# Performance work log

Measured on AMD Instinct MI355X. Metric: run time of the kernel, lower is better.

Reference implementation:

```python
import jax, jax.numpy as jnp
import numpy as np

DIM = 384
HEADS = 12
HEAD_DIM = DIM // HEADS
SCALE = HEAD_DIM ** -0.5
HIDDEN = 4 * DIM
EPS = 1e-5


def _dwconv(x, w, b):
    # depthwise 3x3 conv, NCHW, kernel [C,1,3,3], groups=C
    y = jax.lax.conv_general_dilated(
        x, w, window_strides=(1, 1), padding='SAME',
        dimension_numbers=('NCHW', 'OIHW', 'NCHW'),
        feature_group_count=x.shape[1])
    return y + b[None, :, None, None]


def _layernorm(x, g, b):
    mu = jnp.mean(x, axis=-1, keepdims=True)
    var = jnp.mean(jnp.square(x - mu), axis=-1, keepdims=True)
    return (x - mu) * jax.lax.rsqrt(var + EPS) * g + b


def setup_inputs() -> dict:
    key = jax.random.key(0)
    ks = jax.random.split(key, 10)
    s = 0.02
    inp = {
        'x': jax.random.normal(ks[0], (32, DIM, 28, 28), dtype=jnp.float32),
        'cpe1_w': jax.random.normal(ks[1], (DIM, 1, 3, 3), dtype=jnp.float32) * s,
        'cpe1_b': jnp.zeros((DIM,), jnp.float32),
        'norm1_g': jnp.ones((DIM,), jnp.float32),
        'norm1_b': jnp.zeros((DIM,), jnp.float32),
        'qkv_w': jax.random.normal(ks[2], (3 * DIM, DIM), dtype=jnp.float32) * s,
        'proj_w': jax.random.normal(ks[3], (DIM, DIM), dtype=jnp.float32) * s,
        'proj_b': jnp.zeros((DIM,), jnp.float32),
        'cpe2_w': jax.random.normal(ks[4], (DIM, 1, 3, 3), dtype=jnp.float32) * s,
        'cpe2_b': jnp.zeros((DIM,), jnp.float32),
        'norm2_g': jnp.ones((DIM,), jnp.float32),
        'norm2_b': jnp.zeros((DIM,), jnp.float32),
        'fc1_w': jax.random.normal(ks[5], (HIDDEN, DIM), dtype=jnp.float32) * s,
        'fc1_b': jnp.zeros((HIDDEN,), jnp.float32),
        'fc2_w': jax.random.normal(ks[6], (DIM, HIDDEN), dtype=jnp.float32) * s,
        'fc2_b': jnp.zeros((DIM,), jnp.float32),
    }
    return inp


def reference(x, cpe1_w, cpe1_b, norm1_g, norm1_b, qkv_w, proj_w, proj_b,
              cpe2_w, cpe2_b, norm2_g, norm2_b, fc1_w, fc1_b, fc2_w, fc2_b):
    B, C, H, W = x.shape
    N = H * W
    # cpe1: depthwise conv residual (act = Identity)
    x = x + _dwconv(x, cpe1_w, cpe1_b)
    x = jnp.transpose(x.reshape(B, C, N), (0, 2, 1))  # [B, N, C]

    # channel attention
    cur = _layernorm(x, norm1_g, norm1_b)
    qkv = cur @ qkv_w.T  # [B, N, 3C]
    qkv = qkv.reshape(B, N, 3, HEADS, HEAD_DIM)
    q = qkv[:, :, 0]  # [B, N, h, d]
    k = qkv[:, :, 1] * SCALE
    v = qkv[:, :, 2]
    # attn = k^T @ v over tokens: [B, h, d, d]
    attn = jnp.einsum('bnhd,bnhe->bhde', k, v)
    attn = jax.nn.softmax(attn, axis=-1)
    # out[n,d] = sum_e attn[d,e] * q[n,e]
    out = jnp.einsum('bhde,bnhe->bnhd', attn, q).reshape(B, N, C)
    cur = out @ proj_w.T + proj_b
    x = x + cur

    # cpe2
    x = jnp.transpose(x, (0, 2, 1)).reshape(B, C, H, W)
    x = x + _dwconv(x, cpe2_w, cpe2_b)

    # MLP
    x = jnp.transpose(x.reshape(B, C, N), (0, 2, 1))  # [B, N, C]
    y = _layernorm(x, norm2_g, norm2_b)
    y = jax.nn.gelu(y @ fc1_w.T + fc1_b, approximate=False)
    y = y @ fc2_w.T + fc2_b
    x = x + y
    return jnp.transpose(x, (0, 2, 1)).reshape(B, C, H, W)
```

## Files before the change

kernel.cpp:

```cpp
#include <hip/hip_runtime.h>
#include <hip/hip_bf16.h>

#define CDIM 384
#define NHEADS 12
#define HDIM 32
#define HIDDEN 1536
#define BBATCH 32
#define HH 28
#define WW 28
#define NTOK 784
#define BN (BBATCH * NTOK)
#define LN_EPS 1e-5f
#define ATT_SCALE 0.17677669529663687f
#define YTILES 196
#define PERXCD 25

typedef __hip_bfloat16 bf16;
typedef __attribute__((ext_vector_type(8))) short bf16x8;
typedef __attribute__((ext_vector_type(4))) float f32x4;

__device__ __forceinline__ void stf(float* p, float v) { *p = v; }
__device__ __forceinline__ void stf(bf16* p, float v) { *p = __float2bfloat16(v); }

__device__ __forceinline__ short f2bs(float v) {
    bf16 t = __float2bfloat16(v);
    return *reinterpret_cast<short*>(&t);
}

__device__ __forceinline__ float bf2f(unsigned short u) {
    return __uint_as_float(((unsigned)u) << 16);
}

__device__ __forceinline__ float gelu_f(float x) {
    float u = x * (0.7978845608f + 0.0356774081f * x * x);
    float e = __expf(-2.f * u);
    return x / (1.f + e);
}

__device__ __forceinline__ void gload16(const void* g, void* l) {
    __builtin_amdgcn_global_load_lds(
        (const __attribute__((address_space(1))) unsigned int*)g,
        (__attribute__((address_space(3))) unsigned int*)l, 16, 0, 0);
}

__global__ __launch_bounds__(256) void prep_k(
    const float* __restrict__ w0, const float* __restrict__ w1,
    const float* __restrict__ w2, const float* __restrict__ w3,
    bf16* __restrict__ dst, const float* __restrict__ cw,
    float* __restrict__ cwt)
{
    int blk = blockIdx.x;
    if (blk >= 6912) {
        int i = (blk - 6912) * 256 + threadIdx.x;
        if (i < 9 * CDIM) {
            int k = i / CDIM, c = i % CDIM;
            cwt[i] = cw[c * 9 + k];
        }
        return;
    }
    int i = blk * 256 + threadIdx.x;
    const float* src; int off;
    if (i < 442368)       { src = w0; off = i; }
    else if (i < 589824)  { src = w1; off = i - 442368; }
    else if (i < 1179648) { src = w2; off = i - 589824; }
    else                  { src = w3; off = i - 1179648; }
    dst[i] = __float2bfloat16(src[off]);
}

__global__ __launch_bounds__(256) void cpe1_tr_v3(
    const float* __restrict__ x, const float* __restrict__ w,
    const float* __restrict__ bias, float* __restrict__ xt)
{
    __shared__ float sm[32][130];
    __shared__ float wls[32][10];
    __shared__ float bls[32];
    int b = blockIdx.z;
    int n0 = blockIdx.y * 64;
    int c0 = blockIdx.x * 32;
    int tid = threadIdx.x;
    int nf0 = (n0 - 32) >> 2;

    for (int i = tid; i < 288; i += 256) wls[i / 9][i % 9] = w[c0 * 9 + i];
    if (tid < 32) bls[tid] = bias[c0 + tid];

    const float4* xb = (const float4*)(x + ((size_t)b * CDIM + c0) * NTOK);
#pragma unroll
    for (int i = 0; i < 4; i++) {
        int q = tid + i * 256;
        int row = q >> 5, c4 = q & 31;
        int nf = nf0 + c4;
        float4 v = {0.f, 0.f, 0.f, 0.f};
        if ((unsigned)nf < (NTOK >> 2)) v = xb[(size_t)row * (NTOK >> 2) + nf];
        float2* p = (float2*)&sm[row][c4 * 4];
        p[0] = make_float2(v.x, v.y);
        p[1] = make_float2(v.z, v.w);
    }
    __syncthreads();

    int c = tid & 31;
    int tsub = tid >> 5;
    float wr[9];
#pragma unroll
    for (int k = 0; k < 9; k++) wr[k] = wls[c][k];
    float bb = bls[c];
    const float* s = sm[c];
#pragma unroll
    for (int it = 0; it < 8; it++) {
        int tok = it * 8 + tsub;
        int n = n0 + tok;
        if (n < NTOK) {
            int h = n / WW, wc = n % WW;
            bool hm = h > 0, hp = h < HH - 1, wm = wc > 0, wpv = wc < WW - 1;
            int l = 32 + tok;
            float a = wr[4] * s[l];
            if (hm)        a += wr[1] * s[l - WW];
            if (hp)        a += wr[7] * s[l + WW];
            if (wm)        a += wr[3] * s[l - 1];
            if (wpv)       a += wr[5] * s[l + 1];
            if (hm && wm)  a += wr[0] * s[l - WW - 1];
            if (hm && wpv) a += wr[2] * s[l - WW + 1];
            if (hp && wm)  a += wr[6] * s[l + WW - 1];
            if (hp && wpv) a += wr[8] * s[l + WW + 1];
            xt[((size_t)b * NTOK + n) * CDIM + c0 + c] = s[l] + a + bb;
        }
    }
}

__global__ __launch_bounds__(256) void ln1_k(
    const float* __restrict__ in, const float* __restrict__ g,
    const float* __restrict__ b, bf16* __restrict__ out)
{
    int tid = threadIdx.x;
    int l = tid & 31;
    size_t tok = (size_t)blockIdx.x * 8 + (tid >> 5);
    const float4* row = (const float4*)(in + tok * CDIM);
    float4 v[3];
    float s = 0.f;
#pragma unroll
    for (int j = 0; j < 3; j++) {
        v[j] = row[l + j * 32];
        s += v[j].x + v[j].y + v[j].z + v[j].w;
    }
#pragma unroll
    for (int off = 16; off >= 1; off >>= 1) s += __shfl_xor(s, off);
    float mu = s * (1.f / CDIM);
    float q = 0.f;
#pragma unroll
    for (int j = 0; j < 3; j++) {
        float dx = v[j].x - mu, dy = v[j].y - mu;
        float dz = v[j].z - mu, dw = v[j].w - mu;
        q += dx * dx + dy * dy + dz * dz + dw * dw;
    }
#pragma unroll
    for (int off = 16; off >= 1; off >>= 1) q += __shfl_xor(q, off);
    float rs = rsqrtf(q * (1.f / CDIM) + LN_EPS);
    const float4* g4 = (const float4*)g;
    const float4* b4 = (const float4*)b;
    ushort4* o4 = (ushort4*)(out + tok * CDIM);
#pragma unroll
    for (int j = 0; j < 3; j++) {
        int idx = l + j * 32;
        float4 gv = g4[idx], bv = b4[idx];
        ushort4 r;
        r.x = (unsigned short)f2bs((v[j].x - mu) * rs * gv.x + bv.x);
        r.y = (unsigned short)f2bs((v[j].y - mu) * rs * gv.y + bv.y);
        r.z = (unsigned short)f2bs((v[j].z - mu) * rs * gv.z + bv.z);
        r.w = (unsigned short)f2bs((v[j].w - mu) * rs * gv.w + bv.w);
        o4[idx] = r;
    }
}

__global__ __launch_bounds__(256) void cpe2_ln_fused(
    const float* __restrict__ xin, const float* __restrict__ wt,
    const float* __restrict__ cbias, const float* __restrict__ g,
    const float* __restrict__ b, float* __restrict__ x3,
    bf16* __restrict__ lnout)
{
    __shared__ float wts[9 * CDIM];
    int tid = threadIdx.x;
    for (int i = tid; i < 864; i += 256)
        ((float4*)wts)[i] = ((const float4*)wt)[i];
    __syncthreads();
    int l = tid & 31;
    size_t tok = (size_t)blockIdx.x * 8 + (tid >> 5);
    int n = (int)(tok % NTOK);
    int h = n / WW, wc = n % WW;
    bool hm = h > 0, hp = h < HH - 1, wm = wc > 0, wpv = wc < WW - 1;
    const float* row = xin + tok * CDIM;
    const float4* w4 = (const float4*)wts;
    float4 ctr[3], acc[3];
#pragma unroll
    for (int j = 0; j < 3; j++) {
        int idx = l + j * 32;
        ctr[j] = ((const float4*)row)[idx];
        float4 ww = w4[4 * 96 + idx];
        acc[j].x = ww.x * ctr[j].x; acc[j].y = ww.y * ctr[j].y;
        acc[j].z = ww.z * ctr[j].z; acc[j].w = ww.w * ctr[j].w;
    }
#define TAP(k, cond, dn)                                                     \
    if (cond) {                                                              \
        const float4* rp = (const float4*)(row + (dn) * CDIM);               \
        _Pragma("unroll")                                                    \
        for (int j = 0; j < 3; j++) {                                        \
            int idx = l + j * 32;                                            \
            float4 vv = rp[idx];                                             \
            float4 ww = w4[(k) * 96 + idx];                                  \
            acc[j].x = fmaf(ww.x, vv.x, acc[j].x);                           \
            acc[j].y = fmaf(ww.y, vv.y, acc[j].y);                           \
            acc[j].z = fmaf(ww.z, vv.z, acc[j].z);                           \
            acc[j].w = fmaf(ww.w, vv.w, acc[j].w);                           \
        }                                                                    \
    }
    TAP(0, hm && wm,   -WW - 1)
    TAP(1, hm,         -WW)
    TAP(2, hm && wpv,  -WW + 1)
    TAP(3, wm,         -1)
    TAP(5, wpv,        1)
    TAP(6, hp && wm,   WW - 1)
    TAP(7, hp,         WW)
    TAP(8, hp && wpv,  WW + 1)
#undef TAP
    float s = 0.f;
    float4 val[3];
    float4* x3r = (float4*)(x3 + tok * CDIM);
#pragma unroll
    for (int j = 0; j < 3; j++) {
        int idx = l + j * 32;
        float4 cb = ((const float4*)cbias)[idx];
        val[j].x = ctr[j].x + acc[j].x + cb.x;
        val[j].y = ctr[j].y + acc[j].y + cb.y;
        val[j].z = ctr[j].z + acc[j].z + cb.z;
        val[j].w = ctr[j].w + acc[j].w + cb.w;
        x3r[idx] = val[j];
        s += val[j].x + val[j].y + val[j].z + val[j].w;
    }
#pragma unroll
    for (int off = 16; off >= 1; off >>= 1) s += __shfl_xor(s, off);
    float mu = s * (1.f / CDIM);
    float q = 0.f;
#pragma unroll
    for (int j = 0; j < 3; j++) {
        float dx = val[j].x - mu, dy = val[j].y - mu;
        float dz = val[j].z - mu, dw = val[j].w - mu;
        q += dx * dx + dy * dy + dz * dz + dw * dw;
    }
#pragma unroll
    for (int off = 16; off >= 1; off >>= 1) q += __shfl_xor(q, off);
    float rs = rsqrtf(q * (1.f / CDIM) + LN_EPS);
    const float4* g4 = (const float4*)g;
    const float4* b4 = (const float4*)b;
    ushort4* o4 = (ushort4*)(lnout + tok * CDIM);
#pragma unroll
    for (int j = 0; j < 3; j++) {
        int idx = l + j * 32;
        float4 gv = g4[idx], bv = b4[idx];
        ushort4 r;
        r.x = (unsigned short)f2bs((val[j].x - mu) * rs * gv.x + bv.x);
        r.y = (unsigned short)f2bs((val[j].y - mu) * rs * gv.y + bv.y);
        r.z = (unsigned short)f2bs((val[j].z - mu) * rs * gv.z + bv.z);
        r.w = (unsigned short)f2bs((val[j].w - mu) * rs * gv.w + bv.w);
        o4[idx] = r;
    }
}

template <int ACT, bool RES, typename TO, bool OUTT, int K>
__global__ __launch_bounds__(256, 4) void gemm_mfma(
    const short* __restrict__ Abf, const short* __restrict__ Bw,
    const float* __restrict__ bias, const float* __restrict__ res,
    TO* __restrict__ Co, int M, int NX)
{
    int id = blockIdx.x;
    int xcd = id & 7, slot_ = id >> 3;
    int yloc = slot_ / NX, xx = slot_ - yloc * NX;
    int y = xcd * PERXCD + yloc;
    if (y >= YTILES) return;

    __shared__ __align__(16) short lds[16896];
    const int tid = threadIdx.x;
    const int wid = tid >> 6, lane = tid & 63;
    const int wrow = wid >> 1, wcol = wid & 1;
    const int quad = lane >> 4, lr = lane & 15;
    const int r0 = y * 128, m0 = xx * 128;

    const int srow = lane >> 2;
    const int sg   = (lane & 3) ^ ((lane >> 3) & 3);
    const short* gA = Abf + (size_t)(r0 + wid * 32 + srow) * K + sg * 8;
    const short* gB = Bw  + (size_t)(m0 + wid * 32 + srow) * K + sg * 8;

    auto stage = [&](int k0, int p) {
        short* lA = lds + p * 8192 + wid * 1024;
        short* lB = lds + p * 8192 + 4096 + wid * 1024;
#pragma unroll
        for (int k = 0; k < 2; k++) {
            gload16(gA + k0 + (size_t)k * 16 * K, lA + k * 512);
            gload16(gB + k0 + (size_t)k * 16 * K, lB + k * 512);
        }
    };

    const int slot = (quad ^ ((lr >> 1) & 3)) * 8;
    int fA[4], fB[4];
#pragma unroll
    for (int i = 0; i < 4; i++) {
        fA[i] = (wrow * 64 + i * 16 + lr) * 32 + slot;
        fB[i] = 4096 + (wcol * 64 + i * 16 + lr) * 32 + slot;
    }

    f32x4 acc[4][4] = {};

    stage(0, 0);
    int p = 0;
    for (int k0 = 0; k0 < K; k0 += 32) {
        __syncthreads();
        if (k0 + 32 < K) stage(k0 + 32, p ^ 1);
        const short* As = lds + p * 8192;
        bf16x8 av[4], bv[4];
#pragma unroll
        for (int i = 0; i < 4; i++) {
            av[i] = *(const bf16x8*)(As + fA[i]);
            bv[i] = *(const bf16x8*)(As + fB[i]);
        }
#pragma unroll
        for (int i = 0; i < 4; i++)
#pragma unroll
            for (int j = 0; j < 4; j++)
                acc[i][j] = __builtin_amdgcn_mfma_f32_16x16x32_bf16(
                    av[i], bv[j], acc[i][j], 0, 0, 0);
        p ^= 1;
    }

    if constexpr (OUTT) {
        float* Csf = (float*)lds;
        __syncthreads();
#pragma unroll
        for (int pass = 0; pass < 2; pass++) {
            if (wcol == pass) {
#pragma unroll
                for (int i = 0; i < 4; i++) {
                    int lrow = wrow * 64 + i * 16 + quad * 4;
#pragma unroll
                    for (int j = 0; j < 4; j++) {
                        int lcol = j * 16 + lr;
                        int gc = m0 + pass * 64 + lcol;
                        float bb = bias ? bias[gc] : 0.f;
#pragma unroll
                        for (int rr = 0; rr < 4; rr++) {
                            float v = acc[i][j][rr] + bb;
                            if (RES)
                                v += res[(size_t)(r0 + lrow + rr) * M + gc];
                            if (ACT == 1) v = gelu_f(v);
                            Csf[(lrow + rr) * 66 + lcol] = v;
                        }
                    }
                }
            }
            __syncthreads();
            int tok = tid & 127;
            int csel = tid >> 7;
            int gtok = r0 + tok;
            int bb2 = gtok / NTOK;
            int nn2 = gtok - bb2 * NTOK;
#pragma unroll
            for (int s = 0; s < 32; s++) {
                int cl = s * 2 + csel;
                int gcol = m0 + pass * 64 + cl;
                Co[((size_t)bb2 * CDIM + gcol) * NTOK + nn2] = Csf[tok * 66 + cl];
            }
            __syncthreads();
        }
    } else if constexpr (sizeof(TO) == 4) {
#pragma unroll
        for (int i = 0; i < 4; i++) {
            int gr = r0 + wrow * 64 + i * 16 + quad * 4;
#pragma unroll
            for (int j = 0; j < 4; j++) {
                int gc = m0 + wcol * 64 + j * 16 + lr;
                float bb = bias ? bias[gc] : 0.f;
#pragma unroll
                for (int rr = 0; rr < 4; rr++) {
                    size_t idx = (size_t)(gr + rr) * M + gc;
                    float v = acc[i][j][rr] + bb;
                    if (RES) v += res[idx];
                    if (ACT == 1) v = gelu_f(v);
                    stf((float*)&Co[idx], v);
                }
            }
        }
    } else {
        __syncthreads();
        short* Cs = lds;
#pragma unroll
        for (int i = 0; i < 4; i++) {
            int lrow = wrow * 64 + i * 16 + quad * 4;
#pragma unroll
            for (int j = 0; j < 4; j++) {
                int lcol = wcol * 64 + j * 16 + lr;
                float bb = bias ? bias[m0 + lcol] : 0.f;
#pragma unroll
                for (int rr = 0; rr < 4; rr++) {
                    float v = acc[i][j][rr] + bb;
                    if (ACT == 1) v = gelu_f(v);
                    Cs[(lrow + rr) * 132 + lcol] = f2bs(v);
                }
            }
        }
        __syncthreads();
        short* co = (short*)Co;
#pragma unroll
        for (int s = 0; s < 16; s++) {
            int row = s * 8 + (tid >> 5);
            int seg = tid & 31;
            uint2 vv = *(const uint2*)(Cs + row * 132 + seg * 4);
            *(uint2*)(co + (size_t)(r0 + row) * M + m0 + seg * 4) = vv;
        }
    }
}

__global__ __launch_bounds__(256) void attn_k(
    const bf16* __restrict__ qkv, float* __restrict__ attn)
{
    int bh = blockIdx.x;
    int b = bh / NHEADS, h = bh % NHEADS;
    __shared__ float ks[64][32];
    __shared__ float vs[64][32];
    __shared__ float sm[32][33];
    int tid = threadIdx.x;
    int d = tid >> 3, e0 = (tid & 7) * 4;
    int nn = tid >> 2, q8 = (tid & 3) * 8;
    float acc[4] = {0.f, 0.f, 0.f, 0.f};
    for (int n0 = 0; n0 < NTOK; n0 += 64) {
        int n = n0 + nn;
        float kv[8], vv[8];
        if (n < NTOK) {
            const unsigned short* base =
                (const unsigned short*)qkv + ((size_t)b * NTOK + n) * (3 * CDIM);
            uint4 kq = *(const uint4*)(base + CDIM + h * HDIM + q8);
            uint4 vq = *(const uint4*)(base + 2 * CDIM + h * HDIM + q8);
            const unsigned short* kp = (const unsigned short*)&kq;
            const unsigned short* vp = (const unsigned short*)&vq;
#pragma unroll
            for (int j = 0; j < 8; j++) {
                kv[j] = ATT_SCALE * bf2f(kp[j]);
                vv[j] = bf2f(vp[j]);
            }
        } else {
#pragma unroll
            for (int j = 0; j < 8; j++) { kv[j] = 0.f; vv[j] = 0.f; }
        }
        *(float4*)&ks[nn][q8]     = make_float4(kv[0], kv[1], kv[2], kv[3]);
        *(float4*)&ks[nn][q8 + 4] = make_float4(kv[4], kv[5], kv[6], kv[7]);
        *(float4*)&vs[nn][q8]     = make_float4(vv[0], vv[1], vv[2], vv[3]);
        *(float4*)&vs[nn][q8 + 4] = make_float4(vv[4], vv[5], vv[6], vv[7]);
        __syncthreads();
#pragma unroll 8
        for (int k = 0; k < 64; k++) {
            float kd = ks[k][d];
            float4 vv4 = *(const float4*)&vs[k][e0];
            acc[0] = fmaf(kd, vv4.x, acc[0]);
            acc[1] = fmaf(kd, vv4.y, acc[1]);
            acc[2] = fmaf(kd, vv4.z, acc[2]);
            acc[3] = fmaf(kd, vv4.w, acc[3]);
        }
        __syncthreads();
    }
#pragma unroll
    for (int j = 0; j < 4; j++) sm[d][e0 + j] = acc[j];
    __syncthreads();
    if (tid < 32) {
        float mx = -1e30f;
#pragma unroll
        for (int e = 0; e < 32; e++) mx = fmaxf(mx, sm[tid][e]);
        float ssum = 0.f;
        float ex[32];
#pragma unroll
        for (int e = 0; e < 32; e++) { ex[e] = expf(sm[tid][e] - mx); ssum += ex[e]; }
        float inv = 1.f / ssum;
        float* arow = attn + ((size_t)bh * 32 + tid) * 32;
#pragma unroll
        for (int e = 0; e < 32; e++) arow[e] = ex[e] * inv;
    }
}

__global__ __launch_bounds__(384) void apply_attn_k(
    const bf16* __restrict__ qkv, const float* __restrict__ attn,
    bf16* __restrict__ out)
{
    int b = blockIdx.x;
    int chunk = blockIdx.y;
    int tid = threadIdx.x;
    int h = tid >> 5;
    __shared__ float qs[8][CDIM];
    float at[32];
    const float4* ap = (const float4*)(attn + ((size_t)(b * NHEADS) * 32 + tid) * 32);
#pragma unroll
    for (int e4 = 0; e4 < 8; e4++) {
        float4 v = ap[e4];
        at[e4 * 4 + 0] = v.x; at[e4 * 4 + 1] = v.y;
        at[e4 * 4 + 2] = v.z; at[e4 * 4 + 3] = v.w;
    }
    int row8 = tid / 48;
    int seg = tid - row8 * 48;
    int nbase = chunk * 56;
    for (int t0 = 0; t0 < 56; t0 += 8) {
        __syncthreads();
        {
            int n = nbase + t0 + row8;
            const unsigned short* src =
                (const unsigned short*)qkv + ((size_t)b * NTOK + n) * (3 * CDIM) + seg * 8;
            uint4 qv = *(const uint4*)src;
            const unsigned short* qp = (const unsigned short*)&qv;
            *(float4*)&qs[row8][seg * 8] =
                make_float4(bf2f(qp[0]), bf2f(qp[1]), bf2f(qp[2]), bf2f(qp[3]));
            *(float4*)&qs[row8][seg * 8 + 4] =
                make_float4(bf2f(qp[4]), bf2f(qp[5]), bf2f(qp[6]), bf2f(qp[7]));
        }
        __syncthreads();
#pragma unroll
        for (int i = 0; i < 8; i++) {
            const float4* q4 = (const float4*)&qs[i][h * 32];
            float s = 0.f;
#pragma unroll
            for (int e4 = 0; e4 < 8; e4++) {
                float4 qv = q4[e4];
                s = fmaf(at[e4 * 4 + 0], qv.x, s);
                s = fmaf(at[e4 * 4 + 1], qv.y, s);
                s = fmaf(at[e4 * 4 + 2], qv.z, s);
                s = fmaf(at[e4 * 4 + 3], qv.w, s);
            }
            int n = nbase + t0 + i;
            out[((size_t)b * NTOK + n) * CDIM + tid] = __float2bfloat16(s);
        }
    }
}

extern "C" void kernel_launch(void* const* d_in, const int* in_sizes, int n_in,
                              void* d_out, int out_size, void* d_ws, size_t ws_size,
                              hipStream_t stream) {
    const float* x      = (const float*)d_in[0];
    const float* cpe1_w = (const float*)d_in[1];
    const float* cpe1_b = (const float*)d_in[2];
    const float* n1g    = (const float*)d_in[3];
    const float* n1b    = (const float*)d_in[4];
    const float* qkv_w  = (const float*)d_in[5];
    const float* proj_w = (const float*)d_in[6];
    const float* proj_b = (const float*)d_in[7];
    const float* cpe2_w = (const float*)d_in[8];
    const float* cpe2_b = (const float*)d_in[9];
    const float* n2g    = (const float*)d_in[10];
    const float* n2b    = (const float*)d_in[11];
    const float* fc1_w  = (const float*)d_in[12];
    const float* fc1_b  = (const float*)d_in[13];
    const float* fc2_w  = (const float*)d_in[14];
    const float* fc2_b  = (const float*)d_in[15];

    const size_t A = (size_t)BN * CDIM;
    const size_t HA = A / 2;

    bf16* wqkv  = (bf16*)d_ws;
    bf16* wproj = wqkv + 442368;
    bf16* wfc1  = wproj + 147456;
    bf16* wfc2  = wfc1 + 589824;
    float* base = (float*)d_ws + 884736;

    float* xt        = base;
    bf16*  curb      = (bf16*)(base + A);
    bf16*  ylnb      = (bf16*)(base + A);
    bf16*  qkvb      = (bf16*)(base + A + HA);
    float* x3        = base + A + HA;
    bf16*  h1        = (bf16*)(base + A + HA + A);
    float* attnm     = base + 3 * A;
    bf16*  attn_outb = (bf16*)(base + 3 * A + 393216);
    float* cpe2_wt   = base + (A * 9) / 2;

    const int GEMM_GRID3  = 8 * PERXCD * 3;
    const int GEMM_GRID9  = 8 * PERXCD * 9;
    const int GEMM_GRID12 = 8 * PERXCD * 12;

    prep_k<<<6926, 256, 0, stream>>>(qkv_w, proj_w, fc1_w, fc2_w, wqkv,
                                     cpe2_w, cpe2_wt);

    cpe1_tr_v3<<<dim3(CDIM / 32, 13, BBATCH), 256, 0, stream>>>(
        x, cpe1_w, cpe1_b, xt);
    ln1_k<<<BN / 8, 256, 0, stream>>>(xt, n1g, n1b, curb);
    gemm_mfma<0, false, bf16, false, 384><<<GEMM_GRID9, 256, 0, stream>>>(
        (const short*)curb, (const short*)wqkv, nullptr, nullptr, qkvb, 1152, 9);
    attn_k<<<BBATCH * NHEADS, 256, 0, stream>>>(qkvb, attnm);
    apply_attn_k<<<dim3(BBATCH, 14), 384, 0, stream>>>(qkvb, attnm, attn_outb);
    gemm_mfma<0, true, float, false, 384><<<GEMM_GRID3, 256, 0, stream>>>(
        (const short*)attn_outb, (const short*)wproj, proj_b, xt, xt, 384, 3);
    cpe2_ln_fused<<<BN / 8, 256, 0, stream>>>(xt, cpe2_wt, cpe2_b, n2g, n2b,
                                              x3, ylnb);
    gemm_mfma<1, false, bf16, false, 384><<<GEMM_GRID12, 256, 0, stream>>>(
        (const short*)ylnb, (const short*)wfc1, fc1_b, nullptr, h1, 1536, 12);
    gemm_mfma<0, true, float, true, 1536><<<GEMM_GRID3, 256, 0, stream>>>(
        (const short*)h1, (const short*)wfc2, fc2_b, x3, (float*)d_out, 384, 3);
}
```

Baseline: 402.6 us.

## Use 256x128 tile GEMM with 512 threads for QKV and FC1 projections

Adds a new bf16-output MFMA GEMM kernel that uses 256-row by 128-column tiles, 8 waves per block, double-buffered swizzled LDS staging and an LDS-staged epilogue. The QKV and FC1 GEMMs switch to it, halving the number of row tiles. The aim is more operand reuse per block and less global traffic per FLOP. In exchange, each block needs more registers and LDS, which may lower occupancy, and the tile count drops enough to risk worse load balance across CUs.

```diff
diff --git a/kernel.cpp b/kernel.cpp
--- a/kernel.cpp
+++ b/kernel.cpp
@@ -14,6 +14,8 @@
 #define ATT_SCALE 0.17677669529663687f
 #define YTILES 196
 #define PERXCD 25
+#define YT2 98
+#define PERXCD2 13
 
 typedef __hip_bfloat16 bf16;
 typedef __attribute__((ext_vector_type(8))) short bf16x8;
@@ -260,6 +262,101 @@
         r.z = (unsigned short)f2bs((val[j].z - mu) * rs * gv.z + bv.z);
         r.w = (unsigned short)f2bs((val[j].w - mu) * rs * gv.w + bv.w);
         o4[idx] = r;
+    }
+}
+
+template <int ACT, int K>
+__global__ __launch_bounds__(512, 4) void gemm256(
+    const short* __restrict__ Abf, const short* __restrict__ Bw,
+    const float* __restrict__ bias, bf16* __restrict__ Co, int M, int NX)
+{
+    int id = blockIdx.x;
+    int xcd = id & 7, slot_ = id >> 3;
+    int yloc = slot_ / NX, xx = slot_ - yloc * NX;
+    int y = xcd * PERXCD2 + yloc;
+    if (y >= YT2) return;
+
+    __shared__ __align__(16) short lds[24576];
+    const int tid = threadIdx.x;
+    const int wid = tid >> 6, lane = tid & 63;
+    const int wr = wid >> 1, wc = wid & 1;
+    const int quad = lane >> 4, lr = lane & 15;
+    const int r0 = y * 256, m0 = xx * 128;
+
+    const int srow = lane >> 2;
+    const int sg   = (lane & 3) ^ ((lane >> 3) & 3);
+    const short* gA = Abf + (size_t)(r0 + wid * 32 + srow) * K + sg * 8;
+    const short* gB = Bw  + (size_t)(m0 + wid * 16 + srow) * K + sg * 8;
+
+    auto stage = [&](int k0, int p) {
+        short* lA = lds + p * 12288 + wid * 1024;
+        short* lB = lds + p * 12288 + 8192 + wid * 512;
+#pragma unroll
+        for (int k = 0; k < 2; k++)
+            gload16(gA + k0 + (size_t)k * 16 * K, lA + k * 512);
+        gload16(gB + k0, lB);
+    };
+
+    const int slot = (quad ^ ((lr >> 1) & 3)) * 8;
+    int fA[4], fB[4];
+#pragma unroll
+    for (int i = 0; i < 4; i++) {
+        fA[i] = (wr * 64 + i * 16 + lr) * 32 + slot;
+        fB[i] = 8192 + (wc * 64 + i * 16 + lr) * 32 + slot;
+    }
+
+    f32x4 acc[4][4] = {};
+
+    stage(0, 0);
+    int p = 0;
+    for (int k0 = 0; k0 < K; k0 += 32) {
+        __syncthreads();
+        if (k0 + 32 < K) stage(k0 + 32, p ^ 1);
+        const short* S = lds + p * 12288;
+        bf16x8 av[4], bv[4];
+#pragma unroll
+        for (int i = 0; i < 4; i++) {
+            av[i] = *(const bf16x8*)(S + fA[i]);
+            bv[i] = *(const bf16x8*)(S + fB[i]);
+        }
+#pragma unroll
+        for (int i = 0; i < 4; i++)
+#pragma unroll
+            for (int j = 0; j < 4; j++)
+                acc[i][j] = __builtin_amdgcn_mfma_f32_16x16x32_bf16(
+                    av[i], bv[j], acc[i][j], 0, 0, 0);
+        p ^= 1;
+    }
+
+    __syncthreads();
+    short* slab = lds + wid * 2176;
+    short* co = (short*)Co;
+#pragma unroll
+    for (int sub = 0; sub < 2; sub++) {
+#pragma unroll
+        for (int ii = 0; ii < 2; ii++) {
+            int i = sub * 2 + ii;
+            int srow2 = ii * 16 + quad * 4;
+#pragma unroll
+            for (int j = 0; j < 4; j++) {
+                int scol = j * 16 + lr;
+                float bb = bias ? bias[m0 + wc * 64 + scol] : 0.f;
+#pragma unroll
+                for (int rr = 0; rr < 4; rr++) {
+                    float v = acc[i][j][rr] + bb;
+                    if (ACT == 1) v = gelu_f(v);
+                    slab[(srow2 + rr) * 68 + scol] = f2bs(v);
+                }
+            }
+        }
+#pragma unroll
+        for (int it = 0; it < 8; it++) {
+            int rl = (lane >> 4) + it * 4;
+            int seg = lane & 15;
+            uint2 vv = *(const uint2*)(slab + rl * 68 + seg * 4);
+            int grow = r0 + wr * 64 + sub * 32 + rl;
+            *(uint2*)(co + (size_t)grow * M + m0 + wc * 64 + seg * 4) = vv;
+        }
     }
 }
 
@@ -572,8 +669,8 @@
     float* cpe2_wt   = base + (A * 9) / 2;
 
     const int GEMM_GRID3  = 8 * PERXCD * 3;
-    const int GEMM_GRID9  = 8 * PERXCD * 9;
-    const int GEMM_GRID12 = 8 * PERXCD * 12;
+    const int G256_9  = 8 * PERXCD2 * 9;
+    const int G256_12 = 8 * PERXCD2 * 12;
 
     prep_k<<<6926, 256, 0, stream>>>(qkv_w, proj_w, fc1_w, fc2_w, wqkv,
                                      cpe2_w, cpe2_wt);
@@ -581,16 +678,16 @@
     cpe1_tr_v3<<<dim3(CDIM / 32, 13, BBATCH), 256, 0, stream>>>(
         x, cpe1_w, cpe1_b, xt);
     ln1_k<<<BN / 8, 256, 0, stream>>>(xt, n1g, n1b, curb);
-    gemm_mfma<0, false, bf16, false, 384><<<GEMM_GRID9, 256, 0, stream>>>(
-        (const short*)curb, (const short*)wqkv, nullptr, nullptr, qkvb, 1152, 9);
+    gemm256<0, 384><<<G256_9, 512, 0, stream>>>(
+        (const short*)curb, (const short*)wqkv, nullptr, qkvb, 1152, 9);
     attn_k<<<BBATCH * NHEADS, 256, 0, stream>>>(qkvb, attnm);
     apply_attn_k<<<dim3(BBATCH, 14), 384, 0, stream>>>(qkvb, attnm, attn_outb);
     gemm_mfma<0, true, float, false, 384><<<GEMM_GRID3, 256, 0, stream>>>(
         (const short*)attn_outb, (const short*)wproj, proj_b, xt, xt, 384, 3);
     cpe2_ln_fused<<<BN / 8, 256, 0, stream>>>(xt, cpe2_wt, cpe2_b, n2g, n2b,
                                               x3, ylnb);
-    gemm_mfma<1, false, bf16, false, 384><<<GEMM_GRID12, 256, 0, stream>>>(
-        (const short*)ylnb, (const short*)wfc1, fc1_b, nullptr, h1, 1536, 12);
+    gemm256<1, 384><<<G256_12, 512, 0, stream>>>(
+        (const short*)ylnb, (const short*)wfc1, fc1_b, h1, 1536, 12);
     gemm_mfma<0, true, float, true, 1536><<<GEMM_GRID3, 256, 0, stream>>>(
         (const short*)h1, (const short*)wfc2, fc2_b, x3, (float*)d_out, 384, 3);
 }
```

Result: no change. 403.9 us (+0.3%).

## Split attention k^T·v reduction over token quarters with separate softmax kernel

Applied to the files above, without the earlier changes.

The per-(batch,head) k^T·v accumulation is split into four token ranges of 196, so four times as many blocks run, and each writes partial 32x32 sums to a workspace buffer. A new small kernel adds the four partials and applies the row softmax with one thread per row. The aim is to fill more compute units than the original 384 blocks did, at the cost of an extra launch and partial-sum traffic through global memory.

```diff
diff --git a/kernel.cpp b/kernel.cpp
--- a/kernel.cpp
+++ b/kernel.cpp
@@ -415,22 +415,23 @@
     }
 }
 
-__global__ __launch_bounds__(256) void attn_k(
-    const bf16* __restrict__ qkv, float* __restrict__ attn)
+__global__ __launch_bounds__(256) void attn_part_k(
+    const bf16* __restrict__ qkv, float* __restrict__ part)
 {
     int bh = blockIdx.x;
+    int q4 = blockIdx.y;
     int b = bh / NHEADS, h = bh % NHEADS;
     __shared__ float ks[64][32];
     __shared__ float vs[64][32];
-    __shared__ float sm[32][33];
     int tid = threadIdx.x;
     int d = tid >> 3, e0 = (tid & 7) * 4;
     int nn = tid >> 2, q8 = (tid & 3) * 8;
+    int nstart = q4 * 196, nend = nstart + 196;
     float acc[4] = {0.f, 0.f, 0.f, 0.f};
-    for (int n0 = 0; n0 < NTOK; n0 += 64) {
+    for (int n0 = nstart; n0 < nend; n0 += 64) {
         int n = n0 + nn;
         float kv[8], vv[8];
-        if (n < NTOK) {
+        if (n < nend) {
             const unsigned short* base =
                 (const unsigned short*)qkv + ((size_t)b * NTOK + n) * (3 * CDIM);
             uint4 kq = *(const uint4*)(base + CDIM + h * HDIM + q8);
@@ -462,22 +463,48 @@
         }
         __syncthreads();
     }
-#pragma unroll
-    for (int j = 0; j < 4; j++) sm[d][e0 + j] = acc[j];
-    __syncthreads();
-    if (tid < 32) {
-        float mx = -1e30f;
-#pragma unroll
-        for (int e = 0; e < 32; e++) mx = fmaxf(mx, sm[tid][e]);
-        float ssum = 0.f;
-        float ex[32];
-#pragma unroll
-        for (int e = 0; e < 32; e++) { ex[e] = expf(sm[tid][e] - mx); ssum += ex[e]; }
-        float inv = 1.f / ssum;
-        float* arow = attn + ((size_t)bh * 32 + tid) * 32;
-#pragma unroll
-        for (int e = 0; e < 32; e++) arow[e] = ex[e] * inv;
-    }
+    *(float4*)(part + ((((size_t)q4 * 384) + bh) * 32 + d) * 32 + e0) =
+        make_float4(acc[0], acc[1], acc[2], acc[3]);
+}
+
+__global__ __launch_bounds__(256) void attn_sm_k(
+    const float* __restrict__ part, float* __restrict__ attn)
+{
+    int tid = threadIdx.x;
+    int bh = blockIdx.x * 8 + (tid >> 5);
+    int d = tid & 31;
+    const float4* p0 = (const float4*)(part + ((size_t)bh * 32 + d) * 32);
+    float4 a[8];
+#pragma unroll
+    for (int j = 0; j < 8; j++) a[j] = p0[j];
+#pragma unroll
+    for (int q = 1; q < 4; q++) {
+        const float4* pq = (const float4*)(part + (size_t)q * 393216 +
+                                           ((size_t)bh * 32 + d) * 32);
+#pragma unroll
+        for (int j = 0; j < 8; j++) {
+            float4 v = pq[j];
+            a[j].x += v.x; a[j].y += v.y; a[j].z += v.z; a[j].w += v.w;
+        }
+    }
+    float row[32];
+#pragma unroll
+    for (int j = 0; j < 8; j++) {
+        row[4 * j]     = a[j].x; row[4 * j + 1] = a[j].y;
+        row[4 * j + 2] = a[j].z; row[4 * j + 3] = a[j].w;
+    }
+    float mx = -1e30f;
+#pragma unroll
+    for (int e = 0; e < 32; e++) mx = fmaxf(mx, row[e]);
+    float ssum = 0.f;
+#pragma unroll
+    for (int e = 0; e < 32; e++) { row[e] = expf(row[e] - mx); ssum += row[e]; }
+    float inv = 1.f / ssum;
+    float4* arow = (float4*)(attn + ((size_t)bh * 32 + d) * 32);
+#pragma unroll
+    for (int j = 0; j < 8; j++)
+        arow[j] = make_float4(row[4 * j] * inv, row[4 * j + 1] * inv,
+                              row[4 * j + 2] * inv, row[4 * j + 3] * inv);
 }
 
 __global__ __launch_bounds__(384) void apply_attn_k(
@@ -569,6 +596,7 @@
     bf16*  h1        = (bf16*)(base + A + HA + A);
     float* attnm     = base + 3 * A;
     bf16*  attn_outb = (bf16*)(base + 3 * A + 393216);
+    float* attn_part = base + (A * 7) / 2 + 393216;
     float* cpe2_wt   = base + (A * 9) / 2;
 
     const int GEMM_GRID3  = 8 * PERXCD * 3;
@@ -583,7 +611,8 @@
     ln1_k<<<BN / 8, 256, 0, stream>>>(xt, n1g, n1b, curb);
     gemm_mfma<0, false, bf16, false, 384><<<GEMM_GRID9, 256, 0, stream>>>(
         (const short*)curb, (const short*)wqkv, nullptr, nullptr, qkvb, 1152, 9);
-    attn_k<<<BBATCH * NHEADS, 256, 0, stream>>>(qkvb, attnm);
+    attn_part_k<<<dim3(BBATCH * NHEADS, 4), 256, 0, stream>>>(qkvb, attn_part);
+    attn_sm_k<<<48, 256, 0, stream>>>(attn_part, attnm);
     apply_attn_k<<<dim3(BBATCH, 14), 384, 0, stream>>>(qkvb, attnm, attn_outb);
     gemm_mfma<0, true, float, false, 384><<<GEMM_GRID3, 256, 0, stream>>>(
         (const short*)attn_outb, (const short*)wproj, proj_b, xt, xt, 384, 3);
```

After: 399.7 us. No clear change (-0.7%).
